# Performance work log

Hardware: AMD Instinct MI355X
Metric: run time of the kernel (lower is better)

Reference implementation:

```python
import jax, jax.numpy as jnp
import numpy as np

C = 256          # input_dim
OUT = 256        # output_dim
DM = C // 4      # mamba d_model
DS = 16          # d_state
DC = 4           # d_conv
DI = 2 * DM      # d_inner (expand=2)
DTR = max(1, -(-DM // 16))  # dt_rank = ceil(d_model/16) = 4
B, Dd, H, W = 2, 8, 16, 32


def setup_inputs() -> dict:
    key = jax.random.key(0)
    ks = jax.random.split(key, 12)
    s = 0.02
    inp = {
        'x': jax.random.normal(ks[0], (B, C, Dd, H, W), jnp.float32),
        'ln_g': jnp.ones((C,), jnp.float32),
        'ln_b': jnp.zeros((C,), jnp.float32),
        'in_proj_w': jax.random.normal(ks[1], (2 * DI, DM), jnp.float32) * s,
        'conv_w': jax.random.normal(ks[2], (DI, DC), jnp.float32) * s,
        'conv_b': jnp.zeros((DI,), jnp.float32),
        'x_proj_w': jax.random.normal(ks[3], (DTR + 2 * DS, DI), jnp.float32) * s,
        'dt_proj_w': jax.random.normal(ks[4], (DI, DTR), jnp.float32) * s,
        'dt_proj_b': jax.random.uniform(ks[5], (DI,), jnp.float32, -4.0, -2.0),
        'A_log': jnp.log(jnp.broadcast_to(jnp.arange(1, DS + 1, dtype=jnp.float32), (DI, DS))),
        'D_param': jnp.ones((DI,), jnp.float32),
        'out_proj_w': jax.random.normal(ks[6], (DM, DI), jnp.float32) * s,
        'proj_w': jax.random.normal(ks[7], (OUT, C), jnp.float32) * s,
        'proj_b': jnp.zeros((OUT,), jnp.float32),
        'skip_scale': jnp.ones((1,), jnp.float32),
    }
    return inp


def _layernorm(h, g, b, eps=1e-5):
    mu = jnp.mean(h, axis=-1, keepdims=True)
    var = jnp.mean(jnp.square(h - mu), axis=-1, keepdims=True)
    return (h - mu) * jax.lax.rsqrt(var + eps) * g + b


def _mamba(xp, in_proj_w, conv_w, conv_b, x_proj_w, dt_proj_w, dt_proj_b, A_log, D_param, out_proj_w):
    # xp: (B, L, DM)
    xz = xp @ in_proj_w.T                      # (B, L, 2*DI)
    xc, z = jnp.split(xz, 2, axis=-1)
    # causal depthwise conv1d, kernel DC, left-pad DC-1
    xcT = xc.transpose(0, 2, 1)                # (B, DI, L)
    k = conv_w[:, None, :]                     # (DI, 1, DC)
    conv = jax.lax.conv_general_dilated(xcT, k, (1,), [(DC - 1, 0)], feature_group_count=DI)
    xc = jax.nn.silu(conv + conv_b[None, :, None]).transpose(0, 2, 1)  # (B, L, DI)
    x_dbl = xc @ x_proj_w.T                    # (B, L, DTR+2*DS)
    dt = x_dbl[..., :DTR]
    Bm = x_dbl[..., DTR:DTR + DS]
    Cm = x_dbl[..., DTR + DS:]
    dt = jax.nn.softplus(dt @ dt_proj_w.T + dt_proj_b)  # (B, L, DI)
    A = -jnp.exp(A_log)                        # (DI, DS)
    dA = jnp.exp(dt[..., None] * A)            # (B, L, DI, DS)
    dBx = dt[..., None] * Bm[:, :, None, :] * xc[..., None]  # (B, L, DI, DS)

    def step(h, inp):
        dA_t, dBx_t, C_t = inp
        h = dA_t * h + dBx_t                   # (B, DI, DS)
        y = jnp.einsum('bds,bs->bd', h, C_t)
        return h, y

    h0 = jnp.zeros((xp.shape[0], DI, DS), xp.dtype)
    _, ys = jax.lax.scan(step, h0, (dA.transpose(1, 0, 2, 3), dBx.transpose(1, 0, 2, 3), Cm.transpose(1, 0, 2)))
    y = ys.transpose(1, 0, 2) + D_param * xc   # (B, L, DI)
    y = y * jax.nn.silu(z)
    return y @ out_proj_w.T                    # (B, L, DM)


def reference(x, ln_g, ln_b, in_proj_w, conv_w, conv_b, x_proj_w, dt_proj_w, dt_proj_b,
              A_log, D_param, out_proj_w, proj_w, proj_b, skip_scale):
    Bb, Cc, Dd_, H_, W_ = x.shape
    L = Dd_ * H_ * W_
    xf = x.reshape(Bb, Cc, L).transpose(0, 2, 1)        # (B, L, C)
    xn = _layernorm(xf, ln_g, ln_b)
    parts = xn.reshape(Bb, L, 4, DM).transpose(2, 0, 1, 3)  # (4, B, L, DM), contiguous chunks
    mam = lambda p: _mamba(p, in_proj_w, conv_w, conv_b, x_proj_w, dt_proj_w,
                           dt_proj_b, A_log, D_param, out_proj_w)
    outs = jax.vmap(mam)(parts) + skip_scale * parts    # shared Mamba weights across chunks
    xm = outs.transpose(1, 2, 0, 3).reshape(Bb, L, Cc)
    xm = _layernorm(xm, ln_g, ln_b)                      # same LN module reused
    xp = (xm @ proj_w.T + proj_b).transpose(0, 2, 1)     # (B, OUT, L)
    return xp.reshape(Bb, -1, Dd_, H_, W_)
```

## Files before the change

### kernel.cpp

```cpp
#include <hip/hip_runtime.h>


#define B_    2
#define C_    256
#define L_    4096
#define P_    4
#define DM_   64
#define DI_   128
#define OUT_  256
#define NCH   128
#define CHL   32

__global__ __launch_bounds__(256) void k1_ln(const float* __restrict__ x,
        const float* __restrict__ g, const float* __restrict__ bb,
        float* __restrict__ xn) {
  __shared__ float tile[256][33];
  __shared__ float psum[8][32];
  __shared__ float psq[8][32];
  __shared__ float smu[32], srs[32];
  int t = threadIdx.x;
  int l0 = blockIdx.x * 32;
  int b = blockIdx.y;
  const float* xb = x + (size_t)b * C_ * L_;
  int ll = t & 31, cr = t >> 5;
  for (int i = 0; i < 32; ++i) {
    int c = cr + 8 * i;
    tile[c][ll] = xb[(size_t)c * L_ + l0 + ll];
  }
  __syncthreads();
  {
    int l = t & 31, k = t >> 5;
    float s = 0.f, sq = 0.f;
    #pragma unroll 8
    for (int j = 0; j < 32; ++j) {
      float v = tile[32 * k + j][l];
      s += v; sq += v * v;
    }
    psum[k][l] = s; psq[k][l] = sq;
  }
  __syncthreads();
  if (t < 32) {
    float s = 0.f, sq = 0.f;
    #pragma unroll
    for (int k = 0; k < 8; ++k) { s += psum[k][t]; sq += psq[k][t]; }
    float mu = s * (1.f / 256.f);
    float var = sq * (1.f / 256.f) - mu * mu;
    smu[t] = mu;
    srs[t] = rsqrtf(var + 1e-5f);
  }
  __syncthreads();
  float gc = g[t], bc = bb[t];
  for (int l = 0; l < 32; ++l) {
    float v = (tile[t][l] - smu[l]) * srs[l] * gc + bc;
    xn[((size_t)b * L_ + l0 + l) * C_ + t] = v;
  }
}

__global__ __launch_bounds__(256) void k2_inproj(const float* __restrict__ xn,
        const float* __restrict__ w, float* __restrict__ xz) {
  __shared__ float sa[64 * 68];
  __shared__ float sxz[64 * 68];
  int t = threadIdx.x;
  int row0 = blockIdx.x * 64;
  int o0 = blockIdx.y * 64;
  int bp = row0 >> 12, b = bp >> 2, p = bp & 3, l0 = row0 & 4095;
  #pragma unroll
  for (int i = 0; i < 4; ++i) {
    int idx = t + 256 * i;
    int row = idx >> 4, kq = idx & 15;
    float4 v = *(const float4*)&xn[((size_t)b * L_ + l0 + row) * 256 + p * 64 + kq * 4];
    *(float4*)&sa[row * 68 + kq * 4] = v;
  }
  __syncthreads();
  int l = t & 63;
  int ogu = __builtin_amdgcn_readfirstlane(t >> 6);
  int ob = o0 + ogu * 16;
  float acc[16];
  #pragma unroll
  for (int c = 0; c < 16; ++c) acc[c] = 0.f;
  for (int k4 = 0; k4 < 16; ++k4) {
    float4 a4 = *(const float4*)&sa[l * 68 + k4 * 4];
    const float* wp = w + (size_t)ob * 64 + k4 * 4;
    #pragma unroll
    for (int c = 0; c < 16; ++c) {
      float4 w4 = *(const float4*)&wp[c * 64];
      acc[c] += a4.x * w4.x + a4.y * w4.y + a4.z * w4.z + a4.w * w4.w;
    }
  }
  int ogl = t >> 6;
  #pragma unroll
  for (int c4 = 0; c4 < 4; ++c4) {
    float4 v = make_float4(acc[c4*4+0], acc[c4*4+1], acc[c4*4+2], acc[c4*4+3]);
    *(float4*)&sxz[l * 68 + ogl * 16 + c4 * 4] = v;
  }
  __syncthreads();
  #pragma unroll
  for (int i = 0; i < 4; ++i) {
    int idx = t + 256 * i;
    int row = idx >> 4, cq = idx & 15;
    float4 v = *(const float4*)&sxz[row * 68 + cq * 4];
    *(float4*)&xz[(size_t)(row0 + row) * 256 + o0 + cq * 4] = v;
  }
}

__global__ __launch_bounds__(256) void k3a_conv(const float* __restrict__ xz,
        const float* __restrict__ conv_w, const float* __restrict__ conv_b,
        float* __restrict__ xc) {
  int t = threadIdx.x;
  int d = t & 127, lh = t >> 7;
  int bp = blockIdx.y;
  int lstart = blockIdx.x * 32 + lh * 16;
  const float* xzb = xz + (size_t)bp * L_ * 256;
  float4 cw = *(const float4*)&conv_w[d * 4];
  float cb = conv_b[d];
  float w0 = (lstart >= 3) ? xzb[(size_t)(lstart - 3) * 256 + d] : 0.f;
  float w1 = (lstart >= 2) ? xzb[(size_t)(lstart - 2) * 256 + d] : 0.f;
  float w2 = (lstart >= 1) ? xzb[(size_t)(lstart - 1) * 256 + d] : 0.f;
  const float* xzrow = xzb + (size_t)lstart * 256 + d;
  float* xcrow = xc + ((size_t)bp * L_ + lstart) * 128 + d;
  #pragma unroll 4
  for (int i = 0; i < 16; ++i) {
    float w3 = xzrow[(size_t)i * 256];
    float cv = cb + cw.x * w0 + cw.y * w1 + cw.z * w2 + cw.w * w3;
    float sv = __fdividef(cv, 1.f + __expf(-cv));
    xcrow[(size_t)i * 128] = sv;
    w0 = w1; w1 = w2; w2 = w3;
  }
}

__global__ __launch_bounds__(256) void k3b_xdbl(const float* __restrict__ xc,
        const float* __restrict__ x_proj_w, const float* __restrict__ dt_proj_w,
        const float* __restrict__ dt_proj_b,
        float* __restrict__ bc, float* __restrict__ dt) {
  __shared__ float sa[64 * 132];
  __shared__ float sbc[64 * 33];
  __shared__ float sdb[64 * 8];
  int t = threadIdx.x;
  int row0 = blockIdx.x * 64;
  #pragma unroll
  for (int i = 0; i < 8; ++i) {
    int idx = t + 256 * i;
    int row = idx >> 5, kq = idx & 31;
    float4 v = *(const float4*)&xc[(size_t)(row0 + row) * 128 + kq * 4];
    *(float4*)&sa[row * 132 + kq * 4] = v;
  }
  __syncthreads();
  int l = t & 63;
  int ogu = __builtin_amdgcn_readfirstlane(t >> 6);
  float acc[9];
  #pragma unroll
  for (int rr = 0; rr < 9; ++rr) acc[rr] = 0.f;
  for (int k4 = 0; k4 < 32; ++k4) {
    float4 a4 = *(const float4*)&sa[l * 132 + k4 * 4];
    const float* wp = x_proj_w + (size_t)(ogu * 9) * 128 + k4 * 4;
    #pragma unroll
    for (int rr = 0; rr < 9; ++rr) {
      float4 w4 = *(const float4*)&wp[rr * 128];
      acc[rr] += a4.x * w4.x + a4.y * w4.y + a4.z * w4.z + a4.w * w4.w;
    }
  }
  if (ogu == 0) {
    #pragma unroll
    for (int rr = 0; rr < 4; ++rr) sdb[l * 8 + rr] = acc[rr];
    #pragma unroll
    for (int rr = 4; rr < 9; ++rr) sbc[l * 33 + (rr - 4)] = acc[rr];
  } else {
    #pragma unroll
    for (int rr = 0; rr < 9; ++rr) sbc[l * 33 + (ogu * 9 + rr - 4)] = acc[rr];
  }
  __syncthreads();
  #pragma unroll
  for (int i = 0; i < 8; ++i) {
    int idx = t + 256 * i;
    int row = idx >> 5, col = idx & 31;
    bc[(size_t)(row0 + row) * 32 + col] = sbc[row * 33 + col];
  }
  {
    int d = t & 127, rh = t >> 7;
    float4 dw = *(const float4*)&dt_proj_w[d * 4];
    float dpb = dt_proj_b[d];
    #pragma unroll 4
    for (int i = 0; i < 32; ++i) {
      int row = rh * 32 + i;
      float4 q = *(const float4*)&sdb[row * 8];
      float v = dpb + q.x * dw.x + q.y * dw.y + q.z * dw.z + q.w * dw.w;
      float sp = (v > 20.f) ? v : __logf(1.f + __expf(v));
      dt[(size_t)(row0 + row) * 128 + d] = sp;
    }
  }
}

__global__ __launch_bounds__(128) void k4a_scanA(const float* __restrict__ dt,
        const float* __restrict__ xc, const float* __restrict__ bcbuf,
        const float* __restrict__ A_log,
        float* __restrict__ chA, float* __restrict__ chH) {
  int d = threadIdx.x;
  int ch = blockIdx.x, bp = blockIdx.y;
  float Av[16], h[16];
  #pragma unroll
  for (int q = 0; q < 4; ++q) {
    float4 a = *(const float4*)&A_log[d * 16 + q * 4];
    Av[q*4+0] = -__expf(a.x); Av[q*4+1] = -__expf(a.y);
    Av[q*4+2] = -__expf(a.z); Av[q*4+3] = -__expf(a.w);
  }
  #pragma unroll
  for (int s = 0; s < 16; ++s) h[s] = 0.f;
  float sumdt = 0.f;
  const float* dtp = dt + (size_t)bp * L_ * 128 + (size_t)ch * CHL * 128 + d;
  const float* xcp = xc + (size_t)bp * L_ * 128 + (size_t)ch * CHL * 128 + d;
  const float* bcp = bcbuf + (size_t)bp * L_ * 32 + (size_t)ch * CHL * 32;
  #pragma unroll 2
  for (int tt = 0; tt < CHL; ++tt) {
    float dtv = dtp[tt * 128];
    float xcv = xcp[tt * 128];
    float Bv[16];
    *(float4*)&Bv[0]  = *(const float4*)&bcp[tt * 32 + 0];
    *(float4*)&Bv[4]  = *(const float4*)&bcp[tt * 32 + 4];
    *(float4*)&Bv[8]  = *(const float4*)&bcp[tt * 32 + 8];
    *(float4*)&Bv[12] = *(const float4*)&bcp[tt * 32 + 12];
    float w = dtv * xcv;
    sumdt += dtv;
    #pragma unroll
    for (int s = 0; s < 16; ++s) {
      float dA = __expf(dtv * Av[s]);
      h[s] = fmaf(dA, h[s], w * Bv[s]);
    }
  }
  size_t o = (((size_t)bp * NCH + ch) * 128 + d) * 16;
  #pragma unroll
  for (int s = 0; s < 16; ++s) chA[o + s] = __expf(sumdt * Av[s]);
  #pragma unroll
  for (int s = 0; s < 16; ++s) chH[o + s] = h[s];
}

__global__ __launch_bounds__(256) void k4b1(const float* __restrict__ chA,
        const float* __restrict__ chH, float* __restrict__ pA,
        float* __restrict__ pH) {
  int tid = blockIdx.x * 256 + threadIdx.x;
  int rem = tid & 2047, g = (tid >> 11) & 15, bp = tid >> 15;
  float a = 1.f, h = 0.f;
  #pragma unroll 2
  for (int i = 0; i < 8; ++i) {
    size_t o = ((size_t)(bp * NCH + g * 8 + i)) * 2048 + rem;
    float ca = chA[o], ce = chH[o];
    h = fmaf(ca, h, ce);
    a *= ca;
  }
  pA[tid] = a; pH[tid] = h;
}

__global__ __launch_bounds__(256) void k4b2(const float* __restrict__ pA,
        const float* __restrict__ pH, float* __restrict__ gH) {
  int tid = blockIdx.x * 256 + threadIdx.x;
  int rem = tid & 2047, bp = tid >> 11;
  float h = 0.f;
  for (int g = 0; g < 16; ++g) {
    int o = (bp << 15) + (g << 11) + rem;
    gH[o] = h;
    h = fmaf(pA[o], h, pH[o]);
  }
}

__global__ __launch_bounds__(256) void k4b3(const float* __restrict__ chA,
        float* __restrict__ chH, const float* __restrict__ gH) {
  int tid = blockIdx.x * 256 + threadIdx.x;
  int rem = tid & 2047, g = (tid >> 11) & 15, bp = tid >> 15;
  float h = gH[tid];
  #pragma unroll 2
  for (int i = 0; i < 8; ++i) {
    size_t o = ((size_t)(bp * NCH + g * 8 + i)) * 2048 + rem;
    float a = chA[o], e = chH[o];
    chH[o] = h;
    h = fmaf(a, h, e);
  }
}

__global__ __launch_bounds__(128) void k5_scanB(const float* __restrict__ dt,
        const float* __restrict__ xc, const float* __restrict__ bcbuf,
        const float* __restrict__ xz, const float* __restrict__ A_log,
        const float* __restrict__ D_param, const float* __restrict__ chH,
        float* __restrict__ yg) {
  int d = threadIdx.x;
  int ch = blockIdx.x, bp = blockIdx.y;
  float Av[16], h[16];
  #pragma unroll
  for (int q = 0; q < 4; ++q) {
    float4 a = *(const float4*)&A_log[d * 16 + q * 4];
    Av[q*4+0] = -__expf(a.x); Av[q*4+1] = -__expf(a.y);
    Av[q*4+2] = -__expf(a.z); Av[q*4+3] = -__expf(a.w);
  }
  {
    size_t o = (((size_t)bp * NCH + ch) * 128 + d) * 16;
    #pragma unroll
    for (int q = 0; q < 4; ++q)
      *(float4*)&h[q * 4] = *(const float4*)&chH[o + q * 4];
  }
  float Dv = D_param[d];
  const float* dtp = dt + (size_t)bp * L_ * 128 + (size_t)ch * CHL * 128 + d;
  const float* xcp = xc + (size_t)bp * L_ * 128 + (size_t)ch * CHL * 128 + d;
  const float* bcp = bcbuf + (size_t)bp * L_ * 32 + (size_t)ch * CHL * 32;
  const float* zp  = xz + (size_t)bp * L_ * 256 + (size_t)ch * CHL * 256 + 128 + d;
  float* ygp = yg + (size_t)bp * L_ * 128 + (size_t)ch * CHL * 128 + d;
  #pragma unroll 2
  for (int tt = 0; tt < CHL; ++tt) {
    float dtv = dtp[tt * 128];
    float xcv = xcp[tt * 128];
    float zv  = zp[tt * 256];
    float Bv[16], Cv[16];
    *(float4*)&Bv[0]  = *(const float4*)&bcp[tt * 32 + 0];
    *(float4*)&Bv[4]  = *(const float4*)&bcp[tt * 32 + 4];
    *(float4*)&Bv[8]  = *(const float4*)&bcp[tt * 32 + 8];
    *(float4*)&Bv[12] = *(const float4*)&bcp[tt * 32 + 12];
    *(float4*)&Cv[0]  = *(const float4*)&bcp[tt * 32 + 16];
    *(float4*)&Cv[4]  = *(const float4*)&bcp[tt * 32 + 20];
    *(float4*)&Cv[8]  = *(const float4*)&bcp[tt * 32 + 24];
    *(float4*)&Cv[12] = *(const float4*)&bcp[tt * 32 + 28];
    float w = dtv * xcv;
    float r = 0.f;
    #pragma unroll
    for (int s = 0; s < 16; ++s) {
      float dA = __expf(dtv * Av[s]);
      h[s] = fmaf(dA, h[s], w * Bv[s]);
      r = fmaf(h[s], Cv[s], r);
    }
    float y = fmaf(Dv, xcv, r);
    float sig = __fdividef(1.f, 1.f + __expf(-zv));
    ygp[tt * 128] = y * (zv * sig);
  }
}

__global__ __launch_bounds__(256) void k6a_gemm(const float* __restrict__ yg,
        const float* __restrict__ xn, const float* __restrict__ opw,
        const float* __restrict__ skip, float* __restrict__ xmn) {
  __shared__ float sa[64 * 132];
  __shared__ float sxm[64 * 68];
  int t = threadIdx.x;
  int row0 = blockIdx.x * 64;
  int bp = row0 >> 12, b = bp >> 2, p = bp & 3, l0 = row0 & 4095;
  #pragma unroll
  for (int i = 0; i < 8; ++i) {
    int idx = t + 256 * i;
    int row = idx >> 5, kq = idx & 31;
    float4 v = *(const float4*)&yg[(size_t)(row0 + row) * 128 + kq * 4];
    *(float4*)&sa[row * 132 + kq * 4] = v;
  }
  __syncthreads();
  int l = t & 63;
  int ogu = __builtin_amdgcn_readfirstlane(t >> 6);
  int ob = ogu * 16;
  float acc[16];
  #pragma unroll
  for (int c = 0; c < 16; ++c) acc[c] = 0.f;
  for (int k4 = 0; k4 < 32; ++k4) {
    float4 a4 = *(const float4*)&sa[l * 132 + k4 * 4];
    const float* wp = opw + (size_t)ob * 128 + k4 * 4;
    #pragma unroll
    for (int c = 0; c < 16; ++c) {
      float4 w4 = *(const float4*)&wp[c * 128];
      acc[c] += a4.x * w4.x + a4.y * w4.y + a4.z * w4.z + a4.w * w4.w;
    }
  }
  int ogl = t >> 6;
  #pragma unroll
  for (int c4 = 0; c4 < 4; ++c4) {
    float4 v = make_float4(acc[c4*4+0], acc[c4*4+1], acc[c4*4+2], acc[c4*4+3]);
    *(float4*)&sxm[l * 68 + ogl * 16 + c4 * 4] = v;
  }
  __syncthreads();
  float sk = skip[0];
  #pragma unroll
  for (int i = 0; i < 4; ++i) {
    int idx = t + 256 * i;
    int row = idx >> 4, cq = idx & 15;
    size_t addr = ((size_t)b * L_ + l0 + row) * 256 + p * 64 + cq * 4;
    float4 v = *(const float4*)&sxm[row * 68 + cq * 4];
    float4 xv = *(const float4*)&xn[addr];
    float4 o = make_float4(v.x + sk * xv.x, v.y + sk * xv.y,
                           v.z + sk * xv.z, v.w + sk * xv.w);
    *(float4*)&xmn[addr] = o;
  }
}

__global__ __launch_bounds__(256) void k6ln(float* __restrict__ xmn,
        const float* __restrict__ g, const float* __restrict__ bb) {
  int t = threadIdx.x;
  int row = blockIdx.x * 4 + (t >> 6);
  int lane = t & 63;
  float* rp = xmn + (size_t)row * 256 + lane * 4;
  float4 v = *(const float4*)rp;
  float s = v.x + v.y + v.z + v.w;
  float q = v.x * v.x + v.y * v.y + v.z * v.z + v.w * v.w;
  #pragma unroll
  for (int off = 1; off < 64; off <<= 1) {
    s += __shfl_xor(s, off);
    q += __shfl_xor(q, off);
  }
  float mu = s * (1.f / 256.f);
  float rs = rsqrtf(q * (1.f / 256.f) - mu * mu + 1e-5f);
  float4 g4 = *(const float4*)&g[lane * 4];
  float4 b4 = *(const float4*)&bb[lane * 4];
  float4 o = make_float4((v.x - mu) * rs * g4.x + b4.x,
                         (v.y - mu) * rs * g4.y + b4.y,
                         (v.z - mu) * rs * g4.z + b4.z,
                         (v.w - mu) * rs * g4.w + b4.w);
  *(float4*)rp = o;
}

__global__ __launch_bounds__(256) void k6b_proj(const float* __restrict__ xmn,
        const float* __restrict__ pw, const float* __restrict__ pb,
        float* __restrict__ out) {
  __shared__ float sa[64 * 132];
  int t = threadIdx.x;
  int row0 = blockIdx.x * 64;
  int o0 = blockIdx.y * 64;
  int b = row0 >> 12, l0 = row0 & 4095;
  int l = t & 63;
  int ogu = __builtin_amdgcn_readfirstlane(t >> 6);
  int ob = o0 + ogu * 16;
  float acc[16];
  #pragma unroll
  for (int c = 0; c < 16; ++c) acc[c] = 0.f;
  for (int kt = 0; kt < 2; ++kt) {
    __syncthreads();
    #pragma unroll
    for (int i = 0; i < 8; ++i) {
      int idx = t + 256 * i;
      int row = idx >> 5, kq = idx & 31;
      float4 v = *(const float4*)&xmn[(size_t)(row0 + row) * 256 + kt * 128 + kq * 4];
      *(float4*)&sa[row * 132 + kq * 4] = v;
    }
    __syncthreads();
    for (int k4 = 0; k4 < 32; ++k4) {
      float4 a4 = *(const float4*)&sa[l * 132 + k4 * 4];
      const float* wp = pw + (size_t)ob * 256 + kt * 128 + k4 * 4;
      #pragma unroll
      for (int c = 0; c < 16; ++c) {
        float4 w4 = *(const float4*)&wp[(size_t)c * 256];
        acc[c] += a4.x * w4.x + a4.y * w4.y + a4.z * w4.z + a4.w * w4.w;
      }
    }
  }
  #pragma unroll
  for (int c = 0; c < 16; ++c) {
    int o = ob + c;
    out[((size_t)b * OUT_ + o) * L_ + l0 + l] = acc[c] + pb[o];
  }
}

extern "C" void kernel_launch(void* const* d_in, const int* in_sizes, int n_in,
                              void* d_out, int out_size, void* d_ws, size_t ws_size,
                              hipStream_t stream) {
  (void)in_sizes; (void)n_in; (void)out_size; (void)ws_size;
  const float* x          = (const float*)d_in[0];
  const float* ln_g       = (const float*)d_in[1];
  const float* ln_b       = (const float*)d_in[2];
  const float* in_proj_w  = (const float*)d_in[3];
  const float* conv_w     = (const float*)d_in[4];
  const float* conv_b     = (const float*)d_in[5];
  const float* x_proj_w   = (const float*)d_in[6];
  const float* dt_proj_w  = (const float*)d_in[7];
  const float* dt_proj_b  = (const float*)d_in[8];
  const float* A_log      = (const float*)d_in[9];
  const float* D_param    = (const float*)d_in[10];
  const float* out_proj_w = (const float*)d_in[11];
  const float* proj_w     = (const float*)d_in[12];
  const float* proj_b     = (const float*)d_in[13];
  const float* skip_scale = (const float*)d_in[14];

  float* ws  = (float*)d_ws;
  float* xn  = ws;
  float* xz  = xn + 2097152;
  float* xc  = xz + 8388608;
  float* dt  = xc + 4194304;
  float* bc  = dt + 4194304;
  float* chA = bc + 1048576;
  float* chH = chA + 2097152;
  float* yg  = chH + 2097152;
  float* xmn = yg + 4194304;
  float* pA  = xmn;
  float* pH  = xmn + 262144;
  float* gH  = xmn + 524288;
  float* out = (float*)d_out;

  k1_ln<<<dim3(L_ / 32, B_), 256, 0, stream>>>(x, ln_g, ln_b, xn);
  k2_inproj<<<dim3(512, 4), 256, 0, stream>>>(xn, in_proj_w, xz);
  k3a_conv<<<dim3(128, B_ * P_), 256, 0, stream>>>(xz, conv_w, conv_b, xc);
  k3b_xdbl<<<dim3(512), 256, 0, stream>>>(xc, x_proj_w, dt_proj_w,
      dt_proj_b, bc, dt);
  k4a_scanA<<<dim3(NCH, B_ * P_), 128, 0, stream>>>(dt, xc, bc, A_log, chA, chH);
  k4b1<<<dim3(1024), 256, 0, stream>>>(chA, chH, pA, pH);
  k4b2<<<dim3(64), 256, 0, stream>>>(pA, pH, gH);
  k4b3<<<dim3(1024), 256, 0, stream>>>(chA, chH, gH);
  k5_scanB<<<dim3(NCH, B_ * P_), 128, 0, stream>>>(dt, xc, bc, xz, A_log,
      D_param, chH, yg);
  k6a_gemm<<<dim3(512), 256, 0, stream>>>(yg, xn, out_proj_w, skip_scale, xmn);
  k6ln<<<dim3(B_ * L_ / 4), 256, 0, stream>>>(xmn, ln_g, ln_b);
  k6b_proj<<<dim3(128, 4), 256, 0, stream>>>(xmn, proj_w, proj_b, out);
}
```

Before: 254.4 us.

## Shrink GEMM output tiles, XOR-swizzle shared tiles, and split K into 64-wide chunks

Reworks the four small fp32 GEMM kernels (in_proj, x_proj, out_proj, final proj). Each wave now computes 8 output columns instead of 16, which doubles the grid along the output dimension. The A tile is staged in 64-wide K chunks in an unpadded shared array with an XOR swizzle, which cuts LDS footprint and accumulator registers so more blocks can be resident. The trade-off is that each A row is reloaded once per extra output-column block, and the looped K tiling adds barriers.

```diff
diff --git a/kernel.cpp b/kernel.cpp
--- a/kernel.cpp
+++ b/kernel.cpp
@@ -58,48 +58,47 @@
 
 __global__ __launch_bounds__(256) void k2_inproj(const float* __restrict__ xn,
         const float* __restrict__ w, float* __restrict__ xz) {
-  __shared__ float sa[64 * 68];
-  __shared__ float sxz[64 * 68];
+  __shared__ float sa[64 * 64];
   int t = threadIdx.x;
   int row0 = blockIdx.x * 64;
-  int o0 = blockIdx.y * 64;
+  int o0 = blockIdx.y * 32;
   int bp = row0 >> 12, b = bp >> 2, p = bp & 3, l0 = row0 & 4095;
   #pragma unroll
   for (int i = 0; i < 4; ++i) {
     int idx = t + 256 * i;
     int row = idx >> 4, kq = idx & 15;
     float4 v = *(const float4*)&xn[((size_t)b * L_ + l0 + row) * 256 + p * 64 + kq * 4];
-    *(float4*)&sa[row * 68 + kq * 4] = v;
-  }
-  __syncthreads();
-  int l = t & 63;
-  int ogu = __builtin_amdgcn_readfirstlane(t >> 6);
-  int ob = o0 + ogu * 16;
-  float acc[16];
-  #pragma unroll
-  for (int c = 0; c < 16; ++c) acc[c] = 0.f;
+    *(float4*)&sa[row * 64 + ((kq ^ (row & 15)) << 2)] = v;
+  }
+  __syncthreads();
+  int lane = t & 63;
+  int wid = __builtin_amdgcn_readfirstlane(t >> 6);
+  int ob = o0 + wid * 8;
+  const float* wp0 = w + (size_t)ob * 64;
+  float acc[8];
+  #pragma unroll
+  for (int c = 0; c < 8; ++c) acc[c] = 0.f;
+  #pragma unroll 2
   for (int k4 = 0; k4 < 16; ++k4) {
-    float4 a4 = *(const float4*)&sa[l * 68 + k4 * 4];
-    const float* wp = w + (size_t)ob * 64 + k4 * 4;
-    #pragma unroll
-    for (int c = 0; c < 16; ++c) {
-      float4 w4 = *(const float4*)&wp[c * 64];
+    float4 a4 = *(const float4*)&sa[lane * 64 + ((k4 ^ (lane & 15)) << 2)];
+    #pragma unroll
+    for (int c = 0; c < 8; ++c) {
+      float4 w4 = *(const float4*)&wp0[c * 64 + k4 * 4];
       acc[c] += a4.x * w4.x + a4.y * w4.y + a4.z * w4.z + a4.w * w4.w;
     }
   }
-  int ogl = t >> 6;
-  #pragma unroll
-  for (int c4 = 0; c4 < 4; ++c4) {
-    float4 v = make_float4(acc[c4*4+0], acc[c4*4+1], acc[c4*4+2], acc[c4*4+3]);
-    *(float4*)&sxz[l * 68 + ogl * 16 + c4 * 4] = v;
-  }
-  __syncthreads();
-  #pragma unroll
-  for (int i = 0; i < 4; ++i) {
-    int idx = t + 256 * i;
-    int row = idx >> 4, cq = idx & 15;
-    float4 v = *(const float4*)&sxz[row * 68 + cq * 4];
-    *(float4*)&xz[(size_t)(row0 + row) * 256 + o0 + cq * 4] = v;
+  __syncthreads();
+  int widl = t >> 6;
+  #pragma unroll
+  for (int c = 0; c < 8; ++c) sa[lane * 33 + widl * 8 + c] = acc[c];
+  __syncthreads();
+  {
+    int row = t >> 2, c0 = (t & 3) * 8;
+    float4 v0 = *(const float4*)&sa[row * 33 + c0];
+    float4 v1 = *(const float4*)&sa[row * 33 + c0 + 4];
+    float* op = &xz[(size_t)(row0 + row) * 256 + o0 + c0];
+    *(float4*)op = v0;
+    *(float4*)&op[4] = v1;
   }
 }
 
@@ -132,41 +131,45 @@
         const float* __restrict__ x_proj_w, const float* __restrict__ dt_proj_w,
         const float* __restrict__ dt_proj_b,
         float* __restrict__ bc, float* __restrict__ dt) {
-  __shared__ float sa[64 * 132];
+  __shared__ float sa[64 * 64];
   __shared__ float sbc[64 * 33];
   __shared__ float sdb[64 * 8];
   int t = threadIdx.x;
   int row0 = blockIdx.x * 64;
-  #pragma unroll
-  for (int i = 0; i < 8; ++i) {
-    int idx = t + 256 * i;
-    int row = idx >> 5, kq = idx & 31;
-    float4 v = *(const float4*)&xc[(size_t)(row0 + row) * 128 + kq * 4];
-    *(float4*)&sa[row * 132 + kq * 4] = v;
-  }
-  __syncthreads();
-  int l = t & 63;
-  int ogu = __builtin_amdgcn_readfirstlane(t >> 6);
+  int lane = t & 63;
+  int wid = __builtin_amdgcn_readfirstlane(t >> 6);
+  const float* wbase = x_proj_w + (size_t)(wid * 9) * 128;
   float acc[9];
   #pragma unroll
   for (int rr = 0; rr < 9; ++rr) acc[rr] = 0.f;
-  for (int k4 = 0; k4 < 32; ++k4) {
-    float4 a4 = *(const float4*)&sa[l * 132 + k4 * 4];
-    const float* wp = x_proj_w + (size_t)(ogu * 9) * 128 + k4 * 4;
-    #pragma unroll
-    for (int rr = 0; rr < 9; ++rr) {
-      float4 w4 = *(const float4*)&wp[rr * 128];
-      acc[rr] += a4.x * w4.x + a4.y * w4.y + a4.z * w4.z + a4.w * w4.w;
-    }
-  }
-  if (ogu == 0) {
-    #pragma unroll
-    for (int rr = 0; rr < 4; ++rr) sdb[l * 8 + rr] = acc[rr];
-    #pragma unroll
-    for (int rr = 4; rr < 9; ++rr) sbc[l * 33 + (rr - 4)] = acc[rr];
+  for (int kt = 0; kt < 2; ++kt) {
+    if (kt) __syncthreads();
+    #pragma unroll
+    for (int i = 0; i < 4; ++i) {
+      int idx = t + 256 * i;
+      int row = idx >> 4, kq = idx & 15;
+      float4 v = *(const float4*)&xc[(size_t)(row0 + row) * 128 + kt * 64 + kq * 4];
+      *(float4*)&sa[row * 64 + ((kq ^ (row & 15)) << 2)] = v;
+    }
+    __syncthreads();
+    #pragma unroll 2
+    for (int k4 = 0; k4 < 16; ++k4) {
+      float4 a4 = *(const float4*)&sa[lane * 64 + ((k4 ^ (lane & 15)) << 2)];
+      #pragma unroll
+      for (int rr = 0; rr < 9; ++rr) {
+        float4 w4 = *(const float4*)&wbase[rr * 128 + kt * 64 + k4 * 4];
+        acc[rr] += a4.x * w4.x + a4.y * w4.y + a4.z * w4.z + a4.w * w4.w;
+      }
+    }
+  }
+  if (wid == 0) {
+    #pragma unroll
+    for (int rr = 0; rr < 4; ++rr) sdb[lane * 8 + rr] = acc[rr];
+    #pragma unroll
+    for (int rr = 4; rr < 9; ++rr) sbc[lane * 33 + (rr - 4)] = acc[rr];
   } else {
     #pragma unroll
-    for (int rr = 0; rr < 9; ++rr) sbc[l * 33 + (ogu * 9 + rr - 4)] = acc[rr];
+    for (int rr = 0; rr < 9; ++rr) sbc[lane * 33 + (wid * 9 + rr - 4)] = acc[rr];
   }
   __syncthreads();
   #pragma unroll
@@ -332,52 +335,57 @@
 __global__ __launch_bounds__(256) void k6a_gemm(const float* __restrict__ yg,
         const float* __restrict__ xn, const float* __restrict__ opw,
         const float* __restrict__ skip, float* __restrict__ xmn) {
-  __shared__ float sa[64 * 132];
-  __shared__ float sxm[64 * 68];
+  __shared__ float sa[64 * 64];
   int t = threadIdx.x;
   int row0 = blockIdx.x * 64;
+  int o0 = blockIdx.y * 32;
   int bp = row0 >> 12, b = bp >> 2, p = bp & 3, l0 = row0 & 4095;
-  #pragma unroll
-  for (int i = 0; i < 8; ++i) {
-    int idx = t + 256 * i;
-    int row = idx >> 5, kq = idx & 31;
-    float4 v = *(const float4*)&yg[(size_t)(row0 + row) * 128 + kq * 4];
-    *(float4*)&sa[row * 132 + kq * 4] = v;
-  }
-  __syncthreads();
-  int l = t & 63;
-  int ogu = __builtin_amdgcn_readfirstlane(t >> 6);
-  int ob = ogu * 16;
-  float acc[16];
-  #pragma unroll
-  for (int c = 0; c < 16; ++c) acc[c] = 0.f;
-  for (int k4 = 0; k4 < 32; ++k4) {
-    float4 a4 = *(const float4*)&sa[l * 132 + k4 * 4];
-    const float* wp = opw + (size_t)ob * 128 + k4 * 4;
-    #pragma unroll
-    for (int c = 0; c < 16; ++c) {
-      float4 w4 = *(const float4*)&wp[c * 128];
-      acc[c] += a4.x * w4.x + a4.y * w4.y + a4.z * w4.z + a4.w * w4.w;
-    }
-  }
-  int ogl = t >> 6;
-  #pragma unroll
-  for (int c4 = 0; c4 < 4; ++c4) {
-    float4 v = make_float4(acc[c4*4+0], acc[c4*4+1], acc[c4*4+2], acc[c4*4+3]);
-    *(float4*)&sxm[l * 68 + ogl * 16 + c4 * 4] = v;
-  }
-  __syncthreads();
-  float sk = skip[0];
-  #pragma unroll
-  for (int i = 0; i < 4; ++i) {
-    int idx = t + 256 * i;
-    int row = idx >> 4, cq = idx & 15;
-    size_t addr = ((size_t)b * L_ + l0 + row) * 256 + p * 64 + cq * 4;
-    float4 v = *(const float4*)&sxm[row * 68 + cq * 4];
-    float4 xv = *(const float4*)&xn[addr];
-    float4 o = make_float4(v.x + sk * xv.x, v.y + sk * xv.y,
-                           v.z + sk * xv.z, v.w + sk * xv.w);
-    *(float4*)&xmn[addr] = o;
+  int lane = t & 63;
+  int wid = __builtin_amdgcn_readfirstlane(t >> 6);
+  int ob = o0 + wid * 8;
+  const float* wp0 = opw + (size_t)ob * 128;
+  float acc[8];
+  #pragma unroll
+  for (int c = 0; c < 8; ++c) acc[c] = 0.f;
+  for (int kt = 0; kt < 2; ++kt) {
+    if (kt) __syncthreads();
+    #pragma unroll
+    for (int i = 0; i < 4; ++i) {
+      int idx = t + 256 * i;
+      int row = idx >> 4, kq = idx & 15;
+      float4 v = *(const float4*)&yg[(size_t)(row0 + row) * 128 + kt * 64 + kq * 4];
+      *(float4*)&sa[row * 64 + ((kq ^ (row & 15)) << 2)] = v;
+    }
+    __syncthreads();
+    #pragma unroll 2
+    for (int k4 = 0; k4 < 16; ++k4) {
+      float4 a4 = *(const float4*)&sa[lane * 64 + ((k4 ^ (lane & 15)) << 2)];
+      #pragma unroll
+      for (int c = 0; c < 8; ++c) {
+        float4 w4 = *(const float4*)&wp0[c * 128 + kt * 64 + k4 * 4];
+        acc[c] += a4.x * w4.x + a4.y * w4.y + a4.z * w4.z + a4.w * w4.w;
+      }
+    }
+  }
+  __syncthreads();
+  int widl = t >> 6;
+  #pragma unroll
+  for (int c = 0; c < 8; ++c) sa[lane * 33 + widl * 8 + c] = acc[c];
+  __syncthreads();
+  {
+    float sk = skip[0];
+    int row = t >> 2, c0 = (t & 3) * 8;
+    size_t addr = ((size_t)b * L_ + l0 + row) * 256 + p * 64 + o0 + c0;
+    float4 v0 = *(const float4*)&sa[row * 33 + c0];
+    float4 v1 = *(const float4*)&sa[row * 33 + c0 + 4];
+    float4 x0 = *(const float4*)&xn[addr];
+    float4 x1 = *(const float4*)&xn[addr + 4];
+    float4 o0v = make_float4(v0.x + sk * x0.x, v0.y + sk * x0.y,
+                             v0.z + sk * x0.z, v0.w + sk * x0.w);
+    float4 o1v = make_float4(v1.x + sk * x1.x, v1.y + sk * x1.y,
+                             v1.z + sk * x1.z, v1.w + sk * x1.w);
+    *(float4*)&xmn[addr] = o0v;
+    *(float4*)&xmn[addr + 4] = o1v;
   }
 }
 
@@ -409,41 +417,42 @@
 __global__ __launch_bounds__(256) void k6b_proj(const float* __restrict__ xmn,
         const float* __restrict__ pw, const float* __restrict__ pb,
         float* __restrict__ out) {
-  __shared__ float sa[64 * 132];
+  __shared__ float sa[64 * 64];
   int t = threadIdx.x;
   int row0 = blockIdx.x * 64;
-  int o0 = blockIdx.y * 64;
+  int o0 = blockIdx.y * 32;
   int b = row0 >> 12, l0 = row0 & 4095;
-  int l = t & 63;
-  int ogu = __builtin_amdgcn_readfirstlane(t >> 6);
-  int ob = o0 + ogu * 16;
-  float acc[16];
-  #pragma unroll
-  for (int c = 0; c < 16; ++c) acc[c] = 0.f;
-  for (int kt = 0; kt < 2; ++kt) {
+  int lane = t & 63;
+  int wid = __builtin_amdgcn_readfirstlane(t >> 6);
+  int ob = o0 + wid * 8;
+  const float* wp0 = pw + (size_t)ob * 256;
+  float acc[8];
+  #pragma unroll
+  for (int c = 0; c < 8; ++c) acc[c] = 0.f;
+  for (int kt = 0; kt < 4; ++kt) {
+    if (kt) __syncthreads();
+    #pragma unroll
+    for (int i = 0; i < 4; ++i) {
+      int idx = t + 256 * i;
+      int row = idx >> 4, kq = idx & 15;
+      float4 v = *(const float4*)&xmn[(size_t)(row0 + row) * 256 + kt * 64 + kq * 4];
+      *(float4*)&sa[row * 64 + ((kq ^ (row & 15)) << 2)] = v;
+    }
     __syncthreads();
-    #pragma unroll
-    for (int i = 0; i < 8; ++i) {
-      int idx = t + 256 * i;
-      int row = idx >> 5, kq = idx & 31;
-      float4 v = *(const float4*)&xmn[(size_t)(row0 + row) * 256 + kt * 128 + kq * 4];
-      *(float4*)&sa[row * 132 + kq * 4] = v;
-    }
-    __syncthreads();
-    for (int k4 = 0; k4 < 32; ++k4) {
-      float4 a4 = *(const float4*)&sa[l * 132 + k4 * 4];
-      const float* wp = pw + (size_t)ob * 256 + kt * 128 + k4 * 4;
+    #pragma unroll 2
+    for (int k4 = 0; k4 < 16; ++k4) {
+      float4 a4 = *(const float4*)&sa[lane * 64 + ((k4 ^ (lane & 15)) << 2)];
       #pragma unroll
-      for (int c = 0; c < 16; ++c) {
-        float4 w4 = *(const float4*)&wp[(size_t)c * 256];
+      for (int c = 0; c < 8; ++c) {
+        float4 w4 = *(const float4*)&wp0[c * 256 + kt * 64 + k4 * 4];
         acc[c] += a4.x * w4.x + a4.y * w4.y + a4.z * w4.z + a4.w * w4.w;
       }
     }
   }
   #pragma unroll
-  for (int c = 0; c < 16; ++c) {
+  for (int c = 0; c < 8; ++c) {
     int o = ob + c;
-    out[((size_t)b * OUT_ + o) * L_ + l0 + l] = acc[c] + pb[o];
+    out[((size_t)b * OUT_ + o) * L_ + l0 + lane] = acc[c] + pb[o];
   }
 }
 
@@ -483,7 +492,7 @@
   float* out = (float*)d_out;
 
   k1_ln<<<dim3(L_ / 32, B_), 256, 0, stream>>>(x, ln_g, ln_b, xn);
-  k2_inproj<<<dim3(512, 4), 256, 0, stream>>>(xn, in_proj_w, xz);
+  k2_inproj<<<dim3(512, 8), 256, 0, stream>>>(xn, in_proj_w, xz);
   k3a_conv<<<dim3(128, B_ * P_), 256, 0, stream>>>(xz, conv_w, conv_b, xc);
   k3b_xdbl<<<dim3(512), 256, 0, stream>>>(xc, x_proj_w, dt_proj_w,
       dt_proj_b, bc, dt);
@@ -493,7 +502,7 @@
   k4b3<<<dim3(1024), 256, 0, stream>>>(chA, chH, gH);
   k5_scanB<<<dim3(NCH, B_ * P_), 128, 0, stream>>>(dt, xc, bc, xz, A_log,
       D_param, chH, yg);
-  k6a_gemm<<<dim3(512), 256, 0, stream>>>(yg, xn, out_proj_w, skip_scale, xmn);
+  k6a_gemm<<<dim3(512, 2), 256, 0, stream>>>(yg, xn, out_proj_w, skip_scale, xmn);
   k6ln<<<dim3(B_ * L_ / 4), 256, 0, stream>>>(xmn, ln_g, ln_b);
-  k6b_proj<<<dim3(128, 4), 256, 0, stream>>>(xmn, proj_w, proj_b, out);
-}
+  k6b_proj<<<dim3(128, 8), 256, 0, stream>>>(xmn, proj_w, proj_b, out);
+}
```

Measured after the change: 244.2 us. -4.0%, faster.
